# Performance work log

Hardware: AMD Instinct MI355X
Metric: run time of the kernel (lower is better)

The kernel has to match this reference:

```python
import jax, jax.numpy as jnp
import numpy as np

N = 100000   # nodes
E = 1600000  # edges (avg degree 16)
IN, H, HID, OUT = 128, 2, 64, 32


def setup_inputs() -> dict:
    key = jax.random.key(0)
    ks = jax.random.split(key, 20)
    def p(k, shape, scale=0.1):
        return jax.random.normal(k, shape, jnp.float32) * scale
    inp = {
        "x": jax.random.normal(ks[0], (N, IN), jnp.float32),
        "edge_index": jax.random.randint(ks[1], (2, E), 0, N),
    }
    # per-layer params: W [din, H*dout], att_src/att_dst [H, dout], bias
    dims = [(IN, HID), (H * HID, HID), (H * HID, HID), (H * HID, OUT)]
    for i, (din, dout) in enumerate(dims):
        inp[f"W{i}"] = p(ks[2 + 4 * i], (din, H * dout))
        inp[f"asrc{i}"] = p(ks[3 + 4 * i], (H, dout))
        inp[f"adst{i}"] = p(ks[4 + 4 * i], (H, dout))
        inp[f"b{i}"] = jnp.zeros((H * dout if i < 3 else dout,), jnp.float32)
    return inp


def gat_conv(h, src, dst, W, a_s, a_d, b, concat):
    # PyG GATConv, add_self_loops=False, negative_slope=0.2, eval mode
    heads, dout = a_s.shape
    n = h.shape[0]
    xl = (h @ W).reshape(n, heads, dout)              # [N, H, D]
    alpha_src = jnp.einsum('nhd,hd->nh', xl, a_s)     # [N, H]
    alpha_dst = jnp.einsum('nhd,hd->nh', xl, a_d)
    e = alpha_src[src] + alpha_dst[dst]               # [E, H]
    e = jax.nn.leaky_relu(e, 0.2)
    # segment softmax over edges sharing a destination node
    m = jax.ops.segment_max(e, dst, num_segments=n)
    m = jnp.where(jnp.isfinite(m), m, 0.0)            # guard isolated nodes
    ex = jnp.exp(e - m[dst])
    denom = jax.ops.segment_sum(ex, dst, num_segments=n)
    alpha = ex / (denom[dst] + 1e-16)                 # [E, H]
    msg = xl[src] * alpha[:, :, None]                 # [E, H, D]
    out = jax.ops.segment_sum(msg, dst, num_segments=n)
    out = out.reshape(n, heads * dout) if concat else out.mean(axis=1)
    return out + b


def reference(x, edge_index, W0, asrc0, adst0, b0, W1, asrc1, adst1, b1,
              W2, asrc2, adst2, b2, W3, asrc3, adst3, b3):
    src, dst = edge_index[0], edge_index[1]
    layers = [
        (W0, asrc0, adst0, b0, True),
        (W1, asrc1, adst1, b1, True),
        (W2, asrc2, adst2, b2, True),
        (W3, asrc3, adst3, b3, False),
    ]
    h = x
    for i, (W, a_s, a_d, b, concat) in enumerate(layers):
        h = gat_conv(h, src, dst, W, a_s, a_d, b, concat)
        if i != len(layers) - 1:
            h = jax.nn.relu(h)
    return jax.nn.log_softmax(h, axis=-1)
```

## Files before the change

### kernel.cpp

```cpp
#include <hip/hip_runtime.h>
#include <hip/hip_bf16.h>
#include <math.h>

#define N_NODES 100000
#define N_EDGES 1600000

constexpr int SCAN_B = 1024;

constexpr int BSHIFT = 9, BMASK = 511;
constexpr int NBUCKET = (N_NODES + 511) / 512;
constexpr int BCAP = 16384;
constexpr int CAPB = 12288;
constexpr int EPT = 16, BIN_T = 256, BIN_CHUNK = BIN_T * EPT;

typedef __attribute__((ext_vector_type(8))) short bf16x8;
typedef __attribute__((ext_vector_type(4))) float f32x4;

__device__ __forceinline__ unsigned short f2bf(float f) {
    unsigned int u = __float_as_uint(f);
    unsigned int r = (u + 0x7fff + ((u >> 16) & 1)) >> 16;
    return (unsigned short)r;
}


__global__ __launch_bounds__(BIN_T) void bin_kernel(const int* __restrict__ src,
                                                    const int* __restrict__ dst,
                                                    int* __restrict__ bcnt,
                                                    unsigned int* __restrict__ bstore, int E) {
    __shared__ int cnt[NBUCKET];
    __shared__ int base[NBUCKET];
    int t = threadIdx.x;
    for (int i = t; i < NBUCKET; i += BIN_T) cnt[i] = 0;
    __syncthreads();
    int e0 = blockIdx.x * BIN_CHUNK;
    int ssrc[EPT], sdst[EPT];
#pragma unroll
    for (int k = 0; k < EPT; ++k) {
        int e = e0 + t + k * BIN_T;
        if (e < E) {
            ssrc[k] = src[e];
            sdst[k] = dst[e];
            atomicAdd(&cnt[sdst[k] >> BSHIFT], 1);
        } else {
            sdst[k] = -1;
        }
    }
    __syncthreads();
    for (int i = t; i < NBUCKET; i += BIN_T) {
        base[i] = atomicAdd(&bcnt[i], cnt[i]);
        cnt[i] = 0;
    }
    __syncthreads();
#pragma unroll
    for (int k = 0; k < EPT; ++k) {
        if (sdst[k] >= 0) {
            int b = sdst[k] >> BSHIFT;
            int off = base[b] + atomicAdd(&cnt[b], 1);
            if (off < BCAP)
                bstore[(size_t)b * BCAP + off] =
                    ((unsigned)ssrc[k] << BSHIFT) | (unsigned)(sdst[k] & BMASK);
        }
    }
}

__global__ __launch_bounds__(256) void deg_from_buckets(const int* __restrict__ bcnt,
                                                        const unsigned int* __restrict__ bstore,
                                                        int* __restrict__ deg, int N) {
    __shared__ int dcnt[512];
    int b = blockIdx.x, t = threadIdx.x;
    for (int i = t; i < 512; i += 256) dcnt[i] = 0;
    __syncthreads();
    int cnt = min(bcnt[b], BCAP);
    for (int i = t; i < cnt; i += 256)
        atomicAdd(&dcnt[bstore[(size_t)b * BCAP + i] & BMASK], 1);
    __syncthreads();
    int nodeBase = b << BSHIFT;
    for (int i = t; i < 512; i += 256)
        if (nodeBase + i < N) deg[nodeBase + i] = dcnt[i];
}

__global__ void scan_block_kernel(const int* __restrict__ in, int* __restrict__ out,
                                  int* __restrict__ partials, int n) {
    __shared__ int sh[SCAN_B];
    int gid = blockIdx.x * SCAN_B + threadIdx.x;
    int v = (gid < n) ? in[gid] : 0;
    sh[threadIdx.x] = v;
    __syncthreads();
    for (int off = 1; off < SCAN_B; off <<= 1) {
        int x = (threadIdx.x >= (unsigned)off) ? sh[threadIdx.x - off] : 0;
        __syncthreads();
        sh[threadIdx.x] += x;
        __syncthreads();
    }
    if (gid < n) out[gid] = sh[threadIdx.x];
    if (threadIdx.x == SCAN_B - 1) partials[blockIdx.x] = sh[SCAN_B - 1];
}

__global__ void scan_partials_kernel(int* partials, int nb) {
    __shared__ int sh[SCAN_B];
    int v = (threadIdx.x < (unsigned)nb) ? partials[threadIdx.x] : 0;
    sh[threadIdx.x] = v;
    __syncthreads();
    for (int off = 1; off < SCAN_B; off <<= 1) {
        int x = (threadIdx.x >= (unsigned)off) ? sh[threadIdx.x - off] : 0;
        __syncthreads();
        sh[threadIdx.x] += x;
        __syncthreads();
    }
    if (threadIdx.x < (unsigned)nb) partials[threadIdx.x] = sh[threadIdx.x] - v;
}

__global__ void scan_add_kernel(int* out, const int* __restrict__ partials, int n) {
    int gid = blockIdx.x * SCAN_B + threadIdx.x;
    if (gid < n) out[gid] += partials[blockIdx.x];
}

__global__ __launch_bounds__(256) void build_col_kernel(const int* __restrict__ rp,
                                                        const int* __restrict__ bcnt,
                                                        const unsigned int* __restrict__ bstore,
                                                        int* __restrict__ col, int N) {
    __shared__ int colStage[CAPB];
    __shared__ int rpL[513];
    __shared__ int fillL[512];
    int b = blockIdx.x, t = threadIdx.x;
    int nodeBase = b << BSHIFT;
    int nNodes = min(512, N - nodeBase);
    for (int i = t; i <= nNodes; i += 256) rpL[i] = rp[nodeBase + i];
    for (int i = t; i < nNodes; i += 256) fillL[i] = 0;
    __syncthreads();
    int segBase = rpL[0];
    int segLen = rpL[nNodes] - segBase;
    int cnt = min(bcnt[b], BCAP);
    for (int i = t; i < cnt; i += 256) {
        unsigned e = bstore[(size_t)b * BCAP + i];
        int dl = e & BMASK;
        int sv = (int)(e >> BSHIFT);
        int pos = (rpL[dl] - segBase) + atomicAdd(&fillL[dl], 1);
        if (pos < CAPB) colStage[pos] = sv;
        else col[segBase + pos] = sv;
    }
    __syncthreads();
    int lim = min(segLen, CAPB);
    for (int i = t; i < lim; i += 256) col[segBase + i] = colStage[i];
}

__global__ void transpose_w_kernel(const float* __restrict__ W, unsigned int* __restrict__ Wt, int C) {
    int idx = blockIdx.x * blockDim.x + threadIdx.x;
    if (idx >= C * 64) return;
    int c = idx >> 6, kk = idx & 63;
    float w0 = W[(2 * kk) * C + c];
    float w1 = W[(2 * kk + 1) * C + c];
    Wt[c * 64 + kk] = (unsigned)f2bf(w0) | ((unsigned)f2bf(w1) << 16);
}


template<int HD>
__global__ __launch_bounds__(64) void gemm_alpha_mfma(
    const float* __restrict__ h, const unsigned short* __restrict__ Wt,
    const float* __restrict__ a_s, const float* __restrict__ a_d,
    __hip_bfloat16* __restrict__ xl, float* __restrict__ asrc, float* __restrict__ adst) {
    constexpr int NT = HD / 16;
    constexpr int GR = HD / 4;
    int node0 = blockIdx.x * 16;
    int t = threadIdx.x;
    int lan = t & 15, grp = t >> 4;

    __shared__ unsigned short hb[16][136];
    __shared__ float ob[16][HD + 4];

    const float4* h4 = (const float4*)h;
#pragma unroll
    for (int it = 0; it < 8; ++it) {
        int idx = it * 64 + t;
        int nn = idx >> 5, kk = idx & 31;
        float4 v = h4[(size_t)(node0 + nn) * 32 + kk];
        ushort4 u;
        u.x = f2bf(v.x); u.y = f2bf(v.y); u.z = f2bf(v.z); u.w = f2bf(v.w);
        *(ushort4*)&hb[nn][kk * 4] = u;
    }
    __syncthreads();

    bf16x8 af[4];
#pragma unroll
    for (int ks = 0; ks < 4; ++ks)
        af[ks] = *(const bf16x8*)&hb[lan][ks * 32 + grp * 8];

    f32x4 acc[NT];
#pragma unroll
    for (int i = 0; i < NT; ++i) acc[i] = (f32x4){0.f, 0.f, 0.f, 0.f};

#pragma unroll
    for (int ks = 0; ks < 4; ++ks) {
        bf16x8 bf[NT];
#pragma unroll
        for (int nt = 0; nt < NT; ++nt)
            bf[nt] = *(const bf16x8*)(Wt + (size_t)(nt * 16 + lan) * 128 + ks * 32 + grp * 8);
#pragma unroll
        for (int nt = 0; nt < NT; ++nt)
            acc[nt] = __builtin_amdgcn_mfma_f32_16x16x32_bf16(af[ks], bf[nt], acc[nt], 0, 0, 0);
    }

    float av[NT], dv[NT];
#pragma unroll
    for (int nt = 0; nt < NT; ++nt) {
        av[nt] = a_s[nt * 16 + lan];
        dv[nt] = a_d[nt * 16 + lan];
    }
    float psum[2][4] = {{0.f,0.f,0.f,0.f},{0.f,0.f,0.f,0.f}};
    float pdum[2][4] = {{0.f,0.f,0.f,0.f},{0.f,0.f,0.f,0.f}};
#pragma unroll
    for (int nt = 0; nt < NT; ++nt) {
        int hs = (nt >= NT / 2) ? 1 : 0;
#pragma unroll
        for (int j = 0; j < 4; ++j) {
            psum[hs][j] = fmaf(acc[nt][j], av[nt], psum[hs][j]);
            pdum[hs][j] = fmaf(acc[nt][j], dv[nt], pdum[hs][j]);
        }
    }
#pragma unroll
    for (int off = 1; off <= 8; off <<= 1) {
#pragma unroll
        for (int hs = 0; hs < 2; ++hs)
#pragma unroll
            for (int j = 0; j < 4; ++j) {
                psum[hs][j] += __shfl_xor(psum[hs][j], off, 64);
                pdum[hs][j] += __shfl_xor(pdum[hs][j], off, 64);
            }
    }
    if (lan == 0) {
#pragma unroll
        for (int j = 0; j < 4; ++j) {
            int node = node0 + grp * 4 + j;
            asrc[node * 2 + 0] = psum[0][j];
            asrc[node * 2 + 1] = psum[1][j];
            adst[node * 2 + 0] = pdum[0][j];
            adst[node * 2 + 1] = pdum[1][j];
        }
    }

#pragma unroll
    for (int nt = 0; nt < NT; ++nt)
#pragma unroll
        for (int j = 0; j < 4; ++j)
            ob[grp * 4 + j][nt * 16 + lan] = acc[nt][j];
    __syncthreads();
#pragma unroll
    for (int it = 0; it < 16 * GR / 64; ++it) {
        int idx = it * 64 + t;
        int nn = idx / GR, g = idx % GR;
        float4 v = *(const float4*)&ob[nn][g * 4];
        uint2 u;
        u.x = (unsigned)f2bf(v.x) | ((unsigned)f2bf(v.y) << 16);
        u.y = (unsigned)f2bf(v.z) | ((unsigned)f2bf(v.w) << 16);
        ((uint2*)xl)[(size_t)(node0 + nn) * GR + g] = u;
    }
}


__global__ void aggregate_relu_v4(const __hip_bfloat162* __restrict__ xl2,
                                  const float2* __restrict__ a_src, const float2* __restrict__ a_dst,
                                  const int* __restrict__ rp, const int* __restrict__ col,
                                  const float* __restrict__ bias, float* __restrict__ out) {
    int node = blockIdx.x;
    int t = threadIdx.x;
    int head = t >> 5;
    int beg = rp[node], deg = rp[node + 1] - beg;
    float2 adn = a_dst[node];

    __shared__ int   snS[64];
    __shared__ float pS[2][64];

    float s0 = 0.f, s1 = 0.f;
    float ax0 = 0.f, ay0 = 0.f, ax1 = 0.f, ay1 = 0.f;
    float ax2 = 0.f, ay2 = 0.f, ax3 = 0.f, ay3 = 0.f;

    if (deg <= 64) {
        float e0 = -INFINITY, e1 = -INFINITY;
        if (t < deg) {
            int sn = col[beg + t];
            snS[t] = sn;
            float2 a = a_src[sn];
            e0 = a.x + adn.x; e0 = (e0 >= 0.f) ? e0 : 0.2f * e0;
            e1 = a.y + adn.y; e1 = (e1 >= 0.f) ? e1 : 0.2f * e1;
        }
        float m0 = e0, m1 = e1;
#pragma unroll
        for (int off = 32; off >= 1; off >>= 1) {
            m0 = fmaxf(m0, __shfl_xor(m0, off, 64));
            m1 = fmaxf(m1, __shfl_xor(m1, off, 64));
        }
        if (t < deg) {
            float p0 = __expf(e0 - m0), p1 = __expf(e1 - m1);
            pS[0][t] = p0; pS[1][t] = p1;
            s0 = p0; s1 = p1;
        }
        __syncthreads();
        int j = 0;
        for (; j + 8 <= deg; j += 8) {
            int sa = snS[j+0], sb = snS[j+1], sc = snS[j+2], sd = snS[j+3];
            int se = snS[j+4], sf = snS[j+5], sg = snS[j+6], sh = snS[j+7];
            float pa = pS[head][j+0], pb = pS[head][j+1], pc = pS[head][j+2], pd = pS[head][j+3];
            float pe = pS[head][j+4], pf = pS[head][j+5], pg = pS[head][j+6], ph = pS[head][j+7];
            __hip_bfloat162 va = xl2[(size_t)sa * 64 + t];
            __hip_bfloat162 vb = xl2[(size_t)sb * 64 + t];
            __hip_bfloat162 vc = xl2[(size_t)sc * 64 + t];
            __hip_bfloat162 vd = xl2[(size_t)sd * 64 + t];
            __hip_bfloat162 ve = xl2[(size_t)se * 64 + t];
            __hip_bfloat162 vf = xl2[(size_t)sf * 64 + t];
            __hip_bfloat162 vg = xl2[(size_t)sg * 64 + t];
            __hip_bfloat162 vh = xl2[(size_t)sh * 64 + t];
            ax0 = fmaf(pa, __bfloat162float(va.x), ax0); ay0 = fmaf(pa, __bfloat162float(va.y), ay0);
            ax1 = fmaf(pb, __bfloat162float(vb.x), ax1); ay1 = fmaf(pb, __bfloat162float(vb.y), ay1);
            ax2 = fmaf(pc, __bfloat162float(vc.x), ax2); ay2 = fmaf(pc, __bfloat162float(vc.y), ay2);
            ax3 = fmaf(pd, __bfloat162float(vd.x), ax3); ay3 = fmaf(pd, __bfloat162float(vd.y), ay3);
            ax0 = fmaf(pe, __bfloat162float(ve.x), ax0); ay0 = fmaf(pe, __bfloat162float(ve.y), ay0);
            ax1 = fmaf(pf, __bfloat162float(vf.x), ax1); ay1 = fmaf(pf, __bfloat162float(vf.y), ay1);
            ax2 = fmaf(pg, __bfloat162float(vg.x), ax2); ay2 = fmaf(pg, __bfloat162float(vg.y), ay2);
            ax3 = fmaf(ph, __bfloat162float(vh.x), ax3); ay3 = fmaf(ph, __bfloat162float(vh.y), ay3);
        }
        for (; j < deg; ++j) {
            int sn = snS[j];
            float p = pS[head][j];
            __hip_bfloat162 v = xl2[(size_t)sn * 64 + t];
            ax0 = fmaf(p, __bfloat162float(v.x), ax0);
            ay0 = fmaf(p, __bfloat162float(v.y), ay0);
        }
    } else {
        float m0 = -INFINITY, m1 = -INFINITY;
        for (int j = t; j < deg; j += 64) {
            float2 a = a_src[col[beg + j]];
            float e0 = a.x + adn.x; e0 = (e0 >= 0.f) ? e0 : 0.2f * e0;
            float e1 = a.y + adn.y; e1 = (e1 >= 0.f) ? e1 : 0.2f * e1;
            m0 = fmaxf(m0, e0); m1 = fmaxf(m1, e1);
        }
#pragma unroll
        for (int off = 32; off >= 1; off >>= 1) {
            m0 = fmaxf(m0, __shfl_xor(m0, off, 64));
            m1 = fmaxf(m1, __shfl_xor(m1, off, 64));
        }
        for (int c0 = 0; c0 < deg; c0 += 64) {
            int csz = min(64, deg - c0);
            if (t < csz) {
                int sn = col[beg + c0 + t];
                float2 a = a_src[sn];
                float e0 = a.x + adn.x; e0 = (e0 >= 0.f) ? e0 : 0.2f * e0;
                float e1 = a.y + adn.y; e1 = (e1 >= 0.f) ? e1 : 0.2f * e1;
                float p0 = __expf(e0 - m0), p1 = __expf(e1 - m1);
                snS[t] = sn; pS[0][t] = p0; pS[1][t] = p1;
                s0 += p0; s1 += p1;
            }
            __syncthreads();
            for (int j = 0; j < csz; ++j) {
                int sn = snS[j];
                float p = pS[head][j];
                __hip_bfloat162 v = xl2[(size_t)sn * 64 + t];
                ax0 = fmaf(p, __bfloat162float(v.x), ax0);
                ay0 = fmaf(p, __bfloat162float(v.y), ay0);
            }
            __syncthreads();
        }
    }
#pragma unroll
    for (int off = 32; off >= 1; off >>= 1) {
        s0 += __shfl_xor(s0, off, 64);
        s1 += __shfl_xor(s1, off, 64);
    }
    float s = head ? s1 : s0;
    float inv = 1.0f / (s + 1e-16f);
    float2 b2 = ((const float2*)bias)[t];
    float ox = fmaxf(fmaf(ax0 + ax1 + ax2 + ax3, inv, b2.x), 0.f);
    float oy = fmaxf(fmaf(ay0 + ay1 + ay2 + ay3, inv, b2.y), 0.f);
    ((float2*)out)[(size_t)node * 64 + t] = make_float2(ox, oy);
}

__global__ void aggregate_final_v4(const __hip_bfloat16* __restrict__ xl,
                                   const float2* __restrict__ a_src, const float2* __restrict__ a_dst,
                                   const int* __restrict__ rp, const int* __restrict__ col,
                                   const float* __restrict__ bias, float* __restrict__ out) {
    int node = blockIdx.x;
    int t = threadIdx.x;
    int head = t >> 5;
    int beg = rp[node], deg = rp[node + 1] - beg;
    float2 adn = a_dst[node];

    __shared__ int   snS[64];
    __shared__ float pS[2][64];

    float s0 = 0.f, s1 = 0.f;
    float a0 = 0.f, a1 = 0.f, a2 = 0.f, a3 = 0.f;

    if (deg <= 64) {
        float e0 = -INFINITY, e1 = -INFINITY;
        if (t < deg) {
            int sn = col[beg + t];
            snS[t] = sn;
            float2 a = a_src[sn];
            e0 = a.x + adn.x; e0 = (e0 >= 0.f) ? e0 : 0.2f * e0;
            e1 = a.y + adn.y; e1 = (e1 >= 0.f) ? e1 : 0.2f * e1;
        }
        float m0 = e0, m1 = e1;
#pragma unroll
        for (int off = 32; off >= 1; off >>= 1) {
            m0 = fmaxf(m0, __shfl_xor(m0, off, 64));
            m1 = fmaxf(m1, __shfl_xor(m1, off, 64));
        }
        if (t < deg) {
            float p0 = __expf(e0 - m0), p1 = __expf(e1 - m1);
            pS[0][t] = p0; pS[1][t] = p1;
            s0 = p0; s1 = p1;
        }
        __syncthreads();
        int j = 0;
        for (; j + 8 <= deg; j += 8) {
            int sa = snS[j+0], sb = snS[j+1], sc = snS[j+2], sd = snS[j+3];
            int se = snS[j+4], sf = snS[j+5], sg = snS[j+6], sh = snS[j+7];
            float pa = pS[head][j+0], pb = pS[head][j+1], pc = pS[head][j+2], pd = pS[head][j+3];
            float pe = pS[head][j+4], pf = pS[head][j+5], pg = pS[head][j+6], ph = pS[head][j+7];
            float va = __bfloat162float(xl[(size_t)sa * 64 + t]);
            float vb = __bfloat162float(xl[(size_t)sb * 64 + t]);
            float vc = __bfloat162float(xl[(size_t)sc * 64 + t]);
            float vd = __bfloat162float(xl[(size_t)sd * 64 + t]);
            float ve = __bfloat162float(xl[(size_t)se * 64 + t]);
            float vf = __bfloat162float(xl[(size_t)sf * 64 + t]);
            float vg = __bfloat162float(xl[(size_t)sg * 64 + t]);
            float vh = __bfloat162float(xl[(size_t)sh * 64 + t]);
            a0 = fmaf(pa, va, a0); a1 = fmaf(pb, vb, a1);
            a2 = fmaf(pc, vc, a2); a3 = fmaf(pd, vd, a3);
            a0 = fmaf(pe, ve, a0); a1 = fmaf(pf, vf, a1);
            a2 = fmaf(pg, vg, a2); a3 = fmaf(ph, vh, a3);
        }
        for (; j < deg; ++j) {
            a0 = fmaf(pS[head][j], __bfloat162float(xl[(size_t)snS[j] * 64 + t]), a0);
        }
    } else {
        float m0 = -INFINITY, m1 = -INFINITY;
        for (int j = t; j < deg; j += 64) {
            float2 a = a_src[col[beg + j]];
            float e0 = a.x + adn.x; e0 = (e0 >= 0.f) ? e0 : 0.2f * e0;
            float e1 = a.y + adn.y; e1 = (e1 >= 0.f) ? e1 : 0.2f * e1;
            m0 = fmaxf(m0, e0); m1 = fmaxf(m1, e1);
        }
#pragma unroll
        for (int off = 32; off >= 1; off >>= 1) {
            m0 = fmaxf(m0, __shfl_xor(m0, off, 64));
            m1 = fmaxf(m1, __shfl_xor(m1, off, 64));
        }
        for (int c0 = 0; c0 < deg; c0 += 64) {
            int csz = min(64, deg - c0);
            if (t < csz) {
                int sn = col[beg + c0 + t];
                float2 a = a_src[sn];
                float e0 = a.x + adn.x; e0 = (e0 >= 0.f) ? e0 : 0.2f * e0;
                float e1 = a.y + adn.y; e1 = (e1 >= 0.f) ? e1 : 0.2f * e1;
                float p0 = __expf(e0 - m0), p1 = __expf(e1 - m1);
                snS[t] = sn; pS[0][t] = p0; pS[1][t] = p1;
                s0 += p0; s1 += p1;
            }
            __syncthreads();
            for (int j = 0; j < csz; ++j) {
                a0 = fmaf(pS[head][j], __bfloat162float(xl[(size_t)snS[j] * 64 + t]), a0);
            }
            __syncthreads();
        }
    }
#pragma unroll
    for (int off = 32; off >= 1; off >>= 1) {
        s0 += __shfl_xor(s0, off, 64);
        s1 += __shfl_xor(s1, off, 64);
    }
    float s = head ? s1 : s0;
    float o = (a0 + a1 + a2 + a3) / (s + 1e-16f);
    float other = __shfl_down(o, 32, 64);
    if (t < 32) {
        float v = 0.5f * (o + other) + bias[t];
        float mx = v;
#pragma unroll
        for (int off = 16; off >= 1; off >>= 1) mx = fmaxf(mx, __shfl_xor(mx, off, 32));
        float ex = __expf(v - mx);
        float sm = ex;
#pragma unroll
        for (int off = 16; off >= 1; off >>= 1) sm += __shfl_xor(sm, off, 32);
        out[(size_t)node * 32 + t] = v - mx - logf(sm);
    }
}


extern "C" void kernel_launch(void* const* d_in, const int* in_sizes, int n_in,
                              void* d_out, int out_size, void* d_ws, size_t ws_size,
                              hipStream_t stream) {
    const int N = N_NODES, E = N_EDGES;

    const float* x  = (const float*)d_in[0];
    const int*  ei  = (const int*)d_in[1];
    const float* W0 = (const float*)d_in[2];
    const float* as0 = (const float*)d_in[3];
    const float* ad0 = (const float*)d_in[4];
    const float* b0 = (const float*)d_in[5];
    const float* W1 = (const float*)d_in[6];
    const float* as1 = (const float*)d_in[7];
    const float* ad1 = (const float*)d_in[8];
    const float* b1 = (const float*)d_in[9];
    const float* W2 = (const float*)d_in[10];
    const float* as2 = (const float*)d_in[11];
    const float* ad2 = (const float*)d_in[12];
    const float* b2 = (const float*)d_in[13];
    const float* W3 = (const float*)d_in[14];
    const float* as3 = (const float*)d_in[15];
    const float* ad3 = (const float*)d_in[16];
    const float* b3 = (const float*)d_in[17];
    float* out = (float*)d_out;

    const int* srcv = ei;
    const int* dstv = ei + E;

    char* p = (char*)d_ws;
    auto carve = [&](size_t bytes) -> void* {
        void* r = (void*)p;
        p += (bytes + 255) & ~(size_t)255;
        return r;
    };
    int* deg      = (int*)carve((size_t)N * 4);
    int* rp       = (int*)carve((size_t)(N + 1) * 4);
    int* col      = (int*)carve((size_t)E * 4);
    int* partials = (int*)carve((size_t)SCAN_B * 4);
    int* bcnt     = (int*)carve((size_t)NBUCKET * 4);
    unsigned int* bstore = (unsigned int*)carve((size_t)NBUCKET * BCAP * 4);
    __hip_bfloat16* bufX = (__hip_bfloat16*)carve((size_t)N * 128 * 2);
    float* bufH   = (float*)carve((size_t)N * 128 * 4);
    float* asrc   = (float*)carve((size_t)N * 2 * 4);
    float* adst   = (float*)carve((size_t)N * 2 * 4);
    unsigned short* Wt0 = (unsigned short*)carve((size_t)128 * 128 * 2);
    unsigned short* Wt1 = (unsigned short*)carve((size_t)128 * 128 * 2);
    unsigned short* Wt2 = (unsigned short*)carve((size_t)128 * 128 * 2);
    unsigned short* Wt3 = (unsigned short*)carve((size_t)64 * 128 * 2);

    hipMemsetAsync(bcnt, 0, (size_t)NBUCKET * 4, stream);
    hipMemsetAsync(rp, 0, 4, stream);

    transpose_w_kernel<<<(128 * 64 + 255) / 256, 256, 0, stream>>>(W0, (unsigned int*)Wt0, 128);
    transpose_w_kernel<<<(128 * 64 + 255) / 256, 256, 0, stream>>>(W1, (unsigned int*)Wt1, 128);
    transpose_w_kernel<<<(128 * 64 + 255) / 256, 256, 0, stream>>>(W2, (unsigned int*)Wt2, 128);
    transpose_w_kernel<<<(64 * 64 + 255) / 256, 256, 0, stream>>>(W3, (unsigned int*)Wt3, 64);

    bin_kernel<<<(E + BIN_CHUNK - 1) / BIN_CHUNK, BIN_T, 0, stream>>>(srcv, dstv, bcnt, bstore, E);
    deg_from_buckets<<<NBUCKET, 256, 0, stream>>>(bcnt, bstore, deg, N);
    int nb = (N + SCAN_B - 1) / SCAN_B;
    scan_block_kernel<<<nb, SCAN_B, 0, stream>>>(deg, rp + 1, partials, N);
    scan_partials_kernel<<<1, SCAN_B, 0, stream>>>(partials, nb);
    scan_add_kernel<<<nb, SCAN_B, 0, stream>>>(rp + 1, partials, N);
    build_col_kernel<<<NBUCKET, 256, 0, stream>>>(rp, bcnt, bstore, col, N);

    const __hip_bfloat162* bufX2 = (const __hip_bfloat162*)bufX;
    const float2* asrc2 = (const float2*)asrc;
    const float2* adst2 = (const float2*)adst;

    gemm_alpha_mfma<128><<<N / 16, 64, 0, stream>>>(x, Wt0, as0, ad0, bufX, asrc, adst);
    aggregate_relu_v4<<<N, 64, 0, stream>>>(bufX2, asrc2, adst2, rp, col, b0, bufH);
    gemm_alpha_mfma<128><<<N / 16, 64, 0, stream>>>(bufH, Wt1, as1, ad1, bufX, asrc, adst);
    aggregate_relu_v4<<<N, 64, 0, stream>>>(bufX2, asrc2, adst2, rp, col, b1, bufH);
    gemm_alpha_mfma<128><<<N / 16, 64, 0, stream>>>(bufH, Wt2, as2, ad2, bufX, asrc, adst);
    aggregate_relu_v4<<<N, 64, 0, stream>>>(bufX2, asrc2, adst2, rp, col, b2, bufH);
    gemm_alpha_mfma<64><<<N / 16, 64, 0, stream>>>(bufH, Wt3, as3, ad3, bufX, asrc, adst);
    aggregate_final_v4<<<N, 64, 0, stream>>>(bufX, asrc2, adst2, rp, col, b3, out);
}
```

Measured before the change: 562.1 us.

## Store hidden activations as bf16, fuse CSR build into bucket-local scans, merge weight transposes

Hidden-layer outputs are now written as packed bf16 instead of fp32. The next GEMM loads its MFMA operand fragments straight from global memory, with no conversion pass through shared memory, which halves activation write and read traffic. The CSR build replaces the degree-count kernel and the three-kernel global scan with a single-block scan over bucket counts plus a per-bucket local histogram and scan inside the column-build kernel. The four weight-transpose launches are merged into one. Together these cut launch count and memory traffic, at the cost of the bucket scan assuming NBUCKET ≤ 256 and a final GEMM that reads the last hidden layer in bf16.

```diff
diff --git a/kernel.cpp b/kernel.cpp
--- a/kernel.cpp
+++ b/kernel.cpp
@@ -4,8 +4,6 @@
 
 #define N_NODES 100000
 #define N_EDGES 1600000
-
-constexpr int SCAN_B = 1024;
 
 constexpr int BSHIFT = 9, BMASK = 511;
 constexpr int NBUCKET = (N_NODES + 511) / 512;
@@ -63,100 +61,89 @@
     }
 }
 
-__global__ __launch_bounds__(256) void deg_from_buckets(const int* __restrict__ bcnt,
-                                                        const unsigned int* __restrict__ bstore,
-                                                        int* __restrict__ deg, int N) {
-    __shared__ int dcnt[512];
-    int b = blockIdx.x, t = threadIdx.x;
-    for (int i = t; i < 512; i += 256) dcnt[i] = 0;
-    __syncthreads();
-    int cnt = min(bcnt[b], BCAP);
-    for (int i = t; i < cnt; i += 256)
-        atomicAdd(&dcnt[bstore[(size_t)b * BCAP + i] & BMASK], 1);
-    __syncthreads();
-    int nodeBase = b << BSHIFT;
-    for (int i = t; i < 512; i += 256)
-        if (nodeBase + i < N) deg[nodeBase + i] = dcnt[i];
-}
-
-__global__ void scan_block_kernel(const int* __restrict__ in, int* __restrict__ out,
-                                  int* __restrict__ partials, int n) {
-    __shared__ int sh[SCAN_B];
-    int gid = blockIdx.x * SCAN_B + threadIdx.x;
-    int v = (gid < n) ? in[gid] : 0;
-    sh[threadIdx.x] = v;
-    __syncthreads();
-    for (int off = 1; off < SCAN_B; off <<= 1) {
-        int x = (threadIdx.x >= (unsigned)off) ? sh[threadIdx.x - off] : 0;
+__global__ __launch_bounds__(256) void scan_bcnt_kernel(const int* __restrict__ bcnt,
+                                                        int* __restrict__ bbase) {
+    __shared__ int sh[256];
+    int t = threadIdx.x;
+    int v = (t < NBUCKET) ? min(bcnt[t], BCAP) : 0;
+    sh[t] = v;
+    __syncthreads();
+    for (int off = 1; off < 256; off <<= 1) {
+        int x = (t >= off) ? sh[t - off] : 0;
         __syncthreads();
-        sh[threadIdx.x] += x;
+        sh[t] += x;
         __syncthreads();
     }
-    if (gid < n) out[gid] = sh[threadIdx.x];
-    if (threadIdx.x == SCAN_B - 1) partials[blockIdx.x] = sh[SCAN_B - 1];
-}
-
-__global__ void scan_partials_kernel(int* partials, int nb) {
-    __shared__ int sh[SCAN_B];
-    int v = (threadIdx.x < (unsigned)nb) ? partials[threadIdx.x] : 0;
-    sh[threadIdx.x] = v;
-    __syncthreads();
-    for (int off = 1; off < SCAN_B; off <<= 1) {
-        int x = (threadIdx.x >= (unsigned)off) ? sh[threadIdx.x - off] : 0;
-        __syncthreads();
-        sh[threadIdx.x] += x;
-        __syncthreads();
-    }
-    if (threadIdx.x < (unsigned)nb) partials[threadIdx.x] = sh[threadIdx.x] - v;
-}
-
-__global__ void scan_add_kernel(int* out, const int* __restrict__ partials, int n) {
-    int gid = blockIdx.x * SCAN_B + threadIdx.x;
-    if (gid < n) out[gid] += partials[blockIdx.x];
-}
-
-__global__ __launch_bounds__(256) void build_col_kernel(const int* __restrict__ rp,
-                                                        const int* __restrict__ bcnt,
-                                                        const unsigned int* __restrict__ bstore,
-                                                        int* __restrict__ col, int N) {
+    if (t < NBUCKET) bbase[t + 1] = sh[t];
+    if (t == 0) bbase[0] = 0;
+}
+
+__global__ __launch_bounds__(256) void build_col_v2(const int* __restrict__ bcnt,
+                                                    const int* __restrict__ bbase,
+                                                    const unsigned int* __restrict__ bstore,
+                                                    int* __restrict__ rp, int* __restrict__ col,
+                                                    int N) {
+    __shared__ int sA[512], sB[512];
+    __shared__ int lofs[513];
     __shared__ int colStage[CAPB];
-    __shared__ int rpL[513];
-    __shared__ int fillL[512];
     int b = blockIdx.x, t = threadIdx.x;
     int nodeBase = b << BSHIFT;
     int nNodes = min(512, N - nodeBase);
-    for (int i = t; i <= nNodes; i += 256) rpL[i] = rp[nodeBase + i];
-    for (int i = t; i < nNodes; i += 256) fillL[i] = 0;
-    __syncthreads();
-    int segBase = rpL[0];
-    int segLen = rpL[nNodes] - segBase;
+    for (int i = t; i < 512; i += 256) sA[i] = 0;
+    __syncthreads();
     int cnt = min(bcnt[b], BCAP);
+    size_t sbase = (size_t)b * BCAP;
+    for (int i = t; i < cnt; i += 256) atomicAdd(&sA[bstore[sbase + i] & BMASK], 1);
+    __syncthreads();
+    int* srcp = sA; int* dstp = sB;
+    for (int off = 1; off < 512; off <<= 1) {
+        for (int i = t; i < 512; i += 256) dstp[i] = srcp[i] + ((i >= off) ? srcp[i - off] : 0);
+        __syncthreads();
+        int* tmp = srcp; srcp = dstp; dstp = tmp;
+    }
+    for (int i = t; i < 512; i += 256) lofs[i + 1] = srcp[i];
+    if (t == 0) lofs[0] = 0;
+    for (int i = t; i < 512; i += 256) dstp[i] = 0;
+    __syncthreads();
+    int gbase = bbase[b];
+    for (int i = t; i < nNodes; i += 256) rp[nodeBase + i] = gbase + lofs[i];
+    if (b == NBUCKET - 1 && t == 0) rp[N] = gbase + lofs[nNodes];
     for (int i = t; i < cnt; i += 256) {
-        unsigned e = bstore[(size_t)b * BCAP + i];
+        unsigned e = bstore[sbase + i];
         int dl = e & BMASK;
         int sv = (int)(e >> BSHIFT);
-        int pos = (rpL[dl] - segBase) + atomicAdd(&fillL[dl], 1);
+        int pos = lofs[dl] + atomicAdd(&dstp[dl], 1);
         if (pos < CAPB) colStage[pos] = sv;
-        else col[segBase + pos] = sv;
-    }
-    __syncthreads();
-    int lim = min(segLen, CAPB);
-    for (int i = t; i < lim; i += 256) col[segBase + i] = colStage[i];
-}
-
-__global__ void transpose_w_kernel(const float* __restrict__ W, unsigned int* __restrict__ Wt, int C) {
-    int idx = blockIdx.x * blockDim.x + threadIdx.x;
-    if (idx >= C * 64) return;
-    int c = idx >> 6, kk = idx & 63;
+        else col[gbase + pos] = sv;
+    }
+    __syncthreads();
+    int lim = min(cnt, CAPB);
+    for (int i = t; i < lim; i += 256) col[gbase + i] = colStage[i];
+}
+
+__global__ __launch_bounds__(256) void transpose_all_w(
+    const float* __restrict__ W0, const float* __restrict__ W1,
+    const float* __restrict__ W2, const float* __restrict__ W3,
+    unsigned int* __restrict__ Wt0, unsigned int* __restrict__ Wt1,
+    unsigned int* __restrict__ Wt2, unsigned int* __restrict__ Wt3) {
+    int idx = blockIdx.x * 256 + threadIdx.x;
+    const float* W; unsigned int* Wt; int C, base;
+    if (idx < 8192)       { W = W0; Wt = Wt0; C = 128; base = 0; }
+    else if (idx < 16384) { W = W1; Wt = Wt1; C = 128; base = 8192; }
+    else if (idx < 24576) { W = W2; Wt = Wt2; C = 128; base = 16384; }
+    else if (idx < 28672) { W = W3; Wt = Wt3; C = 64;  base = 24576; }
+    else return;
+    int l = idx - base;
+    int c = l >> 6, kk = l & 63;
     float w0 = W[(2 * kk) * C + c];
     float w1 = W[(2 * kk + 1) * C + c];
     Wt[c * 64 + kk] = (unsigned)f2bf(w0) | ((unsigned)f2bf(w1) << 16);
 }
 
 
-template<int HD>
+template<int HD, bool F32IN>
 __global__ __launch_bounds__(64) void gemm_alpha_mfma(
-    const float* __restrict__ h, const unsigned short* __restrict__ Wt,
+    const void* __restrict__ hsrc, const unsigned short* __restrict__ Wt,
     const float* __restrict__ a_s, const float* __restrict__ a_d,
     __hip_bfloat16* __restrict__ xl, float* __restrict__ asrc, float* __restrict__ adst) {
     constexpr int NT = HD / 16;
@@ -165,25 +152,31 @@
     int t = threadIdx.x;
     int lan = t & 15, grp = t >> 4;
 
-    __shared__ unsigned short hb[16][136];
     __shared__ float ob[16][HD + 4];
 
-    const float4* h4 = (const float4*)h;
-#pragma unroll
-    for (int it = 0; it < 8; ++it) {
-        int idx = it * 64 + t;
-        int nn = idx >> 5, kk = idx & 31;
-        float4 v = h4[(size_t)(node0 + nn) * 32 + kk];
-        ushort4 u;
-        u.x = f2bf(v.x); u.y = f2bf(v.y); u.z = f2bf(v.z); u.w = f2bf(v.w);
-        *(ushort4*)&hb[nn][kk * 4] = u;
-    }
-    __syncthreads();
-
     bf16x8 af[4];
-#pragma unroll
-    for (int ks = 0; ks < 4; ++ks)
-        af[ks] = *(const bf16x8*)&hb[lan][ks * 32 + grp * 8];
+    if constexpr (F32IN) {
+        __shared__ unsigned short hb[16][136];
+        const float4* h4 = (const float4*)hsrc;
+#pragma unroll
+        for (int it = 0; it < 8; ++it) {
+            int idx = it * 64 + t;
+            int nn = idx >> 5, kk = idx & 31;
+            float4 v = h4[(size_t)(node0 + nn) * 32 + kk];
+            ushort4 u;
+            u.x = f2bf(v.x); u.y = f2bf(v.y); u.z = f2bf(v.z); u.w = f2bf(v.w);
+            *(ushort4*)&hb[nn][kk * 4] = u;
+        }
+        __syncthreads();
+#pragma unroll
+        for (int ks = 0; ks < 4; ++ks)
+            af[ks] = *(const bf16x8*)&hb[lan][ks * 32 + grp * 8];
+    } else {
+        const unsigned short* hbf = (const unsigned short*)hsrc;
+#pragma unroll
+        for (int ks = 0; ks < 4; ++ks)
+            af[ks] = *(const bf16x8*)(hbf + (size_t)(node0 + lan) * 128 + ks * 32 + grp * 8);
+    }
 
     f32x4 acc[NT];
 #pragma unroll
@@ -191,13 +184,13 @@
 
 #pragma unroll
     for (int ks = 0; ks < 4; ++ks) {
-        bf16x8 bf[NT];
+        bf16x8 bfr[NT];
 #pragma unroll
         for (int nt = 0; nt < NT; ++nt)
-            bf[nt] = *(const bf16x8*)(Wt + (size_t)(nt * 16 + lan) * 128 + ks * 32 + grp * 8);
+            bfr[nt] = *(const bf16x8*)(Wt + (size_t)(nt * 16 + lan) * 128 + ks * 32 + grp * 8);
 #pragma unroll
         for (int nt = 0; nt < NT; ++nt)
-            acc[nt] = __builtin_amdgcn_mfma_f32_16x16x32_bf16(af[ks], bf[nt], acc[nt], 0, 0, 0);
+            acc[nt] = __builtin_amdgcn_mfma_f32_16x16x32_bf16(af[ks], bfr[nt], acc[nt], 0, 0, 0);
     }
 
     float av[NT], dv[NT];
@@ -257,10 +250,10 @@
 }
 
 
-__global__ void aggregate_relu_v4(const __hip_bfloat162* __restrict__ xl2,
+__global__ void aggregate_relu_v5(const __hip_bfloat162* __restrict__ xl2,
                                   const float2* __restrict__ a_src, const float2* __restrict__ a_dst,
                                   const int* __restrict__ rp, const int* __restrict__ col,
-                                  const float* __restrict__ bias, float* __restrict__ out) {
+                                  const float* __restrict__ bias, unsigned int* __restrict__ out) {
     int node = blockIdx.x;
     int t = threadIdx.x;
     int head = t >> 5;
@@ -370,7 +363,7 @@
     float2 b2 = ((const float2*)bias)[t];
     float ox = fmaxf(fmaf(ax0 + ax1 + ax2 + ax3, inv, b2.x), 0.f);
     float oy = fmaxf(fmaf(ay0 + ay1 + ay2 + ay3, inv, b2.y), 0.f);
-    ((float2*)out)[(size_t)node * 64 + t] = make_float2(ox, oy);
+    out[(size_t)node * 64 + t] = (unsigned)f2bf(ox) | ((unsigned)f2bf(oy) << 16);
 }
 
 __global__ void aggregate_final_v4(const __hip_bfloat16* __restrict__ xl,
@@ -519,14 +512,13 @@
         p += (bytes + 255) & ~(size_t)255;
         return r;
     };
-    int* deg      = (int*)carve((size_t)N * 4);
     int* rp       = (int*)carve((size_t)(N + 1) * 4);
     int* col      = (int*)carve((size_t)E * 4);
-    int* partials = (int*)carve((size_t)SCAN_B * 4);
     int* bcnt     = (int*)carve((size_t)NBUCKET * 4);
+    int* bbase    = (int*)carve((size_t)(NBUCKET + 1) * 4);
     unsigned int* bstore = (unsigned int*)carve((size_t)NBUCKET * BCAP * 4);
     __hip_bfloat16* bufX = (__hip_bfloat16*)carve((size_t)N * 128 * 2);
-    float* bufH   = (float*)carve((size_t)N * 128 * 4);
+    __hip_bfloat16* bufH = (__hip_bfloat16*)carve((size_t)N * 128 * 2);
     float* asrc   = (float*)carve((size_t)N * 2 * 4);
     float* adst   = (float*)carve((size_t)N * 2 * 4);
     unsigned short* Wt0 = (unsigned short*)carve((size_t)128 * 128 * 2);
@@ -535,31 +527,25 @@
     unsigned short* Wt3 = (unsigned short*)carve((size_t)64 * 128 * 2);
 
     hipMemsetAsync(bcnt, 0, (size_t)NBUCKET * 4, stream);
-    hipMemsetAsync(rp, 0, 4, stream);
-
-    transpose_w_kernel<<<(128 * 64 + 255) / 256, 256, 0, stream>>>(W0, (unsigned int*)Wt0, 128);
-    transpose_w_kernel<<<(128 * 64 + 255) / 256, 256, 0, stream>>>(W1, (unsigned int*)Wt1, 128);
-    transpose_w_kernel<<<(128 * 64 + 255) / 256, 256, 0, stream>>>(W2, (unsigned int*)Wt2, 128);
-    transpose_w_kernel<<<(64 * 64 + 255) / 256, 256, 0, stream>>>(W3, (unsigned int*)Wt3, 64);
+
+    transpose_all_w<<<112, 256, 0, stream>>>(W0, W1, W2, W3,
+                                             (unsigned int*)Wt0, (unsigned int*)Wt1,
+                                             (unsigned int*)Wt2, (unsigned int*)Wt3);
 
     bin_kernel<<<(E + BIN_CHUNK - 1) / BIN_CHUNK, BIN_T, 0, stream>>>(srcv, dstv, bcnt, bstore, E);
-    deg_from_buckets<<<NBUCKET, 256, 0, stream>>>(bcnt, bstore, deg, N);
-    int nb = (N + SCAN_B - 1) / SCAN_B;
-    scan_block_kernel<<<nb, SCAN_B, 0, stream>>>(deg, rp + 1, partials, N);
-    scan_partials_kernel<<<1, SCAN_B, 0, stream>>>(partials, nb);
-    scan_add_kernel<<<nb, SCAN_B, 0, stream>>>(rp + 1, partials, N);
-    build_col_kernel<<<NBUCKET, 256, 0, stream>>>(rp, bcnt, bstore, col, N);
+    scan_bcnt_kernel<<<1, 256, 0, stream>>>(bcnt, bbase);
+    build_col_v2<<<NBUCKET, 256, 0, stream>>>(bcnt, bbase, bstore, rp, col, N);
 
     const __hip_bfloat162* bufX2 = (const __hip_bfloat162*)bufX;
     const float2* asrc2 = (const float2*)asrc;
     const float2* adst2 = (const float2*)adst;
 
-    gemm_alpha_mfma<128><<<N / 16, 64, 0, stream>>>(x, Wt0, as0, ad0, bufX, asrc, adst);
-    aggregate_relu_v4<<<N, 64, 0, stream>>>(bufX2, asrc2, adst2, rp, col, b0, bufH);
-    gemm_alpha_mfma<128><<<N / 16, 64, 0, stream>>>(bufH, Wt1, as1, ad1, bufX, asrc, adst);
-    aggregate_relu_v4<<<N, 64, 0, stream>>>(bufX2, asrc2, adst2, rp, col, b1, bufH);
-    gemm_alpha_mfma<128><<<N / 16, 64, 0, stream>>>(bufH, Wt2, as2, ad2, bufX, asrc, adst);
-    aggregate_relu_v4<<<N, 64, 0, stream>>>(bufX2, asrc2, adst2, rp, col, b2, bufH);
-    gemm_alpha_mfma<64><<<N / 16, 64, 0, stream>>>(bufH, Wt3, as3, ad3, bufX, asrc, adst);
+    gemm_alpha_mfma<128, true><<<N / 16, 64, 0, stream>>>(x, Wt0, as0, ad0, bufX, asrc, adst);
+    aggregate_relu_v5<<<N, 64, 0, stream>>>(bufX2, asrc2, adst2, rp, col, b0, (unsigned int*)bufH);
+    gemm_alpha_mfma<128, false><<<N / 16, 64, 0, stream>>>(bufH, Wt1, as1, ad1, bufX, asrc, adst);
+    aggregate_relu_v5<<<N, 64, 0, stream>>>(bufX2, asrc2, adst2, rp, col, b1, (unsigned int*)bufH);
+    gemm_alpha_mfma<128, false><<<N / 16, 64, 0, stream>>>(bufH, Wt2, as2, ad2, bufX, asrc, adst);
+    aggregate_relu_v5<<<N, 64, 0, stream>>>(bufX2, asrc2, adst2, rp, col, b2, (unsigned int*)bufH);
+    gemm_alpha_mfma<64, false><<<N / 16, 64, 0, stream>>>(bufH, Wt3, as3, ad3, bufX, asrc, adst);
     aggregate_final_v4<<<N, 64, 0, stream>>>(bufX, asrc2, adst2, rp, col, b3, out);
 }
```

Result: faster. 532.7 us (-5.2%).
